# Kernel optimization log

Hardware: AMD Instinct MI355X
Metric: run time of the kernel (lower is better)

Reference implementation:

```python
import jax, jax.numpy as jnp
import numpy as np

N = 50000
E = 640000
F_IN = 128
HID = 128
OUT = 64


def setup_inputs() -> dict:
    key = jax.random.key(0)
    ks = jax.random.split(key, 16)
    x = jax.random.normal(ks[0], (N, F_IN), dtype=jnp.float32)
    edge_index = jax.random.randint(ks[1], (2, E), 0, N, dtype=jnp.int64)

    def lin(k, fan_in, fan_out):
        bound = 1.0 / np.sqrt(fan_in)
        kw, kb = jax.random.split(k)
        W = jax.random.uniform(kw, (fan_in, fan_out), jnp.float32, -bound, bound)
        b = jax.random.uniform(kb, (fan_out,), jnp.float32, -bound, bound)
        return W, b

    W1, b1 = lin(ks[2], F_IN, HID)
    W2, b2 = lin(ks[3], HID, HID)
    W3, b3 = lin(ks[4], HID, HID)
    Wres, bres = lin(ks[5], F_IN, HID)
    Wlin, blin = lin(ks[6], HID, OUT)
    return {"x": x, "edge_index": edge_index,
            "W1": W1, "b1": b1, "W2": W2, "b2": b2, "W3": W3, "b3": b3,
            "Wres": Wres, "bres": bres, "Wlin": Wlin, "blin": blin}


def _gcn_norm(edge_index, n):
    # GCNConv default: add self-loops, symmetric normalization D^-1/2 (A+I) D^-1/2
    src, dst = edge_index[0], edge_index[1]
    deg = jax.ops.segment_sum(jnp.ones((edge_index.shape[1],), jnp.float32), dst,
                              num_segments=n) + 1.0  # +1 for self-loop
    dinv = jax.lax.rsqrt(deg)
    norm_e = dinv[src] * dinv[dst]          # [E] edge coefficients
    norm_self = 1.0 / deg                    # [N] self-loop coefficients
    return src, dst, norm_e, norm_self


def _gcn_conv(x, W, b, src, dst, norm_e, norm_self, n):
    h = x @ W                                # [N, F_out]
    agg = jax.ops.segment_sum(h[src] * norm_e[:, None], dst, num_segments=n)
    agg = agg + h * norm_self[:, None]       # self-loop contribution
    return agg + b


def reference(x, edge_index, W1, b1, W2, b2, W3, b3, Wres, bres, Wlin, blin):
    n = x.shape[0]
    src, dst, norm_e, norm_self = _gcn_norm(edge_index, n)
    x_res = x @ Wres + bres
    h = _gcn_conv(x, W1, b1, src, dst, norm_e, norm_self, n)
    h = jax.nn.relu(h + x_res)               # dropout is identity in eval mode
    h = _gcn_conv(h, W2, b2, src, dst, norm_e, norm_self, n)
    h = jax.nn.relu(h)
    h = _gcn_conv(h, W3, b3, src, dst, norm_e, norm_self, n)
    h = jax.nn.relu(h)
    return h @ Wlin + blin
```

## Files before the change

### kernel.cpp

```cpp
#include <hip/hip_runtime.h>

typedef unsigned short ushort_t;
typedef unsigned int uint_t;

typedef __bf16 bf16x8 __attribute__((ext_vector_type(8)));
typedef float f32x4 __attribute__((ext_vector_type(4)));

union BFU { ushort_t u; __bf16 h; };

__device__ __forceinline__ float bf2f(uint_t u) {
    union { uint_t i; float f; } v; v.i = u << 16; return v.f;
}
__device__ __forceinline__ ushort_t f2bf(float f) {
    union { float f; uint_t i; } v; v.f = f;
    uint_t r = v.i + 0x7fffu + ((v.i >> 16) & 1u);
    return (ushort_t)(r >> 16);
}
__device__ __forceinline__ float loadF(const void* p, size_t i, int isBf16) {
    return isBf16 ? bf2f((uint_t)((const ushort_t*)p)[i]) : ((const float*)p)[i];
}

struct DetectArgs {
    const void* t[11];
    int elems[11];
    const int* ei;
    int* flags;
};

__global__ void k_init(DetectArgs a, int* __restrict__ deg, int n) {
    int i = blockIdx.x * blockDim.x + threadIdx.x;
    if (i < n) deg[i] = 0;
    if (blockIdx.x == 0) {
        int t = threadIdx.x;
        if (t < 11) {
            const uint_t* w = (const uint_t*)a.t[t];
            int m = a.elems[t] / 2; if (m > 64) m = 64;
            int cnt = 0;
            for (int k = 0; k < m; ++k) {
                uint_t field = (w[k] >> 7) & 0xFFu;
                cnt += (field >= 100u && field <= 135u);
            }
            a.flags[t] = (cnt * 10 >= m * 6) ? 1 : 0;
        } else if (t == 11) {
            int nz = 0;
            for (int k = 0; k < 64; ++k) nz += (a.ei[2 * k + 1] != 0);
            a.flags[11] = (nz == 0) ? 1 : 0;
        }
    }
}

__global__ void k_deg(const int* __restrict__ ei, int E, int N,
                      const int* __restrict__ flags, int* __restrict__ deg) {
    int i = blockIdx.x * blockDim.x + threadIdx.x;
    int e0 = i * 4;
    if (e0 >= E) return;
    int is64 = flags[11];
    if (e0 + 3 < E && (E & 3) == 0) {
        int d[4];
        if (is64) {
            int4 va = *(const int4*)(ei + 2 * E + 2 * e0);
            int4 vb = *(const int4*)(ei + 2 * E + 2 * e0 + 4);
            d[0] = va.x; d[1] = va.z; d[2] = vb.x; d[3] = vb.z;
        } else {
            int4 va = *(const int4*)(ei + E + e0);
            d[0] = va.x; d[1] = va.y; d[2] = va.z; d[3] = va.w;
        }
#pragma unroll
        for (int k = 0; k < 4; ++k)
            if ((unsigned)d[k] < (unsigned)N) atomicAdd(&deg[d[k]], 1);
    } else {
        for (int e = e0; e < E && e < e0 + 4; ++e) {
            int dd = is64 ? ei[2 * E + 2 * e] : ei[E + e];
            if ((unsigned)dd < (unsigned)N) atomicAdd(&deg[dd], 1);
        }
    }
}


__global__ __launch_bounds__(256) void k_bsum(const int* __restrict__ deg, int n,
                                              int* __restrict__ bsum) {
    int base = blockIdx.x * 1024;
    int local = 0;
#pragma unroll
    for (int j = 0; j < 4; ++j) {
        int idx = base + threadIdx.x + j * 256;
        if (idx < n) local += deg[idx];
    }
    __shared__ int s[4];
#pragma unroll
    for (int off = 32; off; off >>= 1) local += __shfl_down(local, off, 64);
    if ((threadIdx.x & 63) == 0) s[threadIdx.x >> 6] = local;
    __syncthreads();
    if (threadIdx.x == 0) bsum[blockIdx.x] = s[0] + s[1] + s[2] + s[3];
}

__global__ __launch_bounds__(256) void k_bscan(int* __restrict__ bsum, int nb) {
    __shared__ int s[256];
    int t = threadIdx.x;
    int v = (t < nb) ? bsum[t] : 0;
    s[t] = v;
    __syncthreads();
    for (int off = 1; off < 256; off <<= 1) {
        int u = (t >= off) ? s[t - off] : 0;
        __syncthreads();
        s[t] += u;
        __syncthreads();
    }
    if (t < nb) bsum[t] = s[t] - v;
}

__global__ __launch_bounds__(256) void k_rowptr(const int* __restrict__ deg,
                                                const int* __restrict__ boff, int n,
                                                int* __restrict__ row_ptr,
                                                int* __restrict__ cnt,
                                                float* __restrict__ dinv,
                                                float* __restrict__ nself) {
    __shared__ int s[256];
    int t = threadIdx.x;
    int base = blockIdx.x * 1024 + t * 4;
    int v0 = (base + 0 < n) ? deg[base + 0] : 0;
    int v1 = (base + 1 < n) ? deg[base + 1] : 0;
    int v2 = (base + 2 < n) ? deg[base + 2] : 0;
    int v3 = (base + 3 < n) ? deg[base + 3] : 0;
    int tot = v0 + v1 + v2 + v3;
    s[t] = tot;
    __syncthreads();
    for (int off = 1; off < 256; off <<= 1) {
        int u = (t >= off) ? s[t - off] : 0;
        __syncthreads();
        s[t] += u;
        __syncthreads();
    }
    int run = boff[blockIdx.x] + ((t == 0) ? 0 : s[t - 1]);
    int vals[4] = {v0, v1, v2, v3};
#pragma unroll
    for (int j = 0; j < 4; ++j) {
        int idx = base + j;
        if (idx < n) {
            row_ptr[idx] = run;
            cnt[idx] = run;
            run += vals[j];
            float df = (float)vals[j] + 1.0f;
            dinv[idx] = rsqrtf(df);
            nself[idx] = 1.0f / df;
        }
    }
    if (blockIdx.x == gridDim.x - 1 && t == 255) row_ptr[n] = boff[blockIdx.x] + s[255];
}

__global__ void k_fill(const int* __restrict__ ei, int E, int N,
                       const int* __restrict__ flags,
                       int* __restrict__ cnt,
                       const float* __restrict__ dinv,
                       uint2* __restrict__ colwgt) {
    int i = blockIdx.x * blockDim.x + threadIdx.x;
    int e0 = i * 4;
    if (e0 >= E) return;
    int is64 = flags[11];
    if (e0 + 3 < E && (E & 3) == 0) {
        int s[4], d[4];
        if (is64) {
            int4 sa = *(const int4*)(ei + 2 * e0);
            int4 sb = *(const int4*)(ei + 2 * e0 + 4);
            int4 da = *(const int4*)(ei + 2 * E + 2 * e0);
            int4 db = *(const int4*)(ei + 2 * E + 2 * e0 + 4);
            s[0] = sa.x; s[1] = sa.z; s[2] = sb.x; s[3] = sb.z;
            d[0] = da.x; d[1] = da.z; d[2] = db.x; d[3] = db.z;
        } else {
            int4 sa = *(const int4*)(ei + e0);
            int4 da = *(const int4*)(ei + E + e0);
            s[0] = sa.x; s[1] = sa.y; s[2] = sa.z; s[3] = sa.w;
            d[0] = da.x; d[1] = da.y; d[2] = da.z; d[3] = da.w;
        }
        float wv[4]; int pos[4]; int ss[4]; bool ok[4];
#pragma unroll
        for (int k = 0; k < 4; ++k) {
            ok[k] = (unsigned)d[k] < (unsigned)N;
            ss[k] = ((unsigned)s[k] < (unsigned)N) ? s[k] : 0;
        }
#pragma unroll
        for (int k = 0; k < 4; ++k)
            wv[k] = ok[k] ? dinv[ss[k]] * dinv[d[k]] : 0.0f;
#pragma unroll
        for (int k = 0; k < 4; ++k)
            pos[k] = ok[k] ? atomicAdd(&cnt[d[k]], 1) : 0;
#pragma unroll
        for (int k = 0; k < 4; ++k) {
            if (ok[k]) {
                uint2 pk;
                pk.x = (uint_t)ss[k];
                pk.y = __float_as_uint(wv[k]);
                colwgt[pos[k]] = pk;
            }
        }
    } else {
        for (int e = e0; e < E && e < e0 + 4; ++e) {
            int sv = is64 ? ei[2 * e] : ei[e];
            int dv = is64 ? ei[2 * E + 2 * e] : ei[E + e];
            if ((unsigned)dv < (unsigned)N) {
                int pos = atomicAdd(&cnt[dv], 1);
                int ssv = ((unsigned)sv < (unsigned)N) ? sv : 0;
                uint2 pk;
                pk.x = (uint_t)ssv;
                pk.y = __float_as_uint(dinv[ssv] * dinv[dv]);
                colwgt[pos] = pk;
            }
        }
    }
}

__global__ void k_pack(const void* __restrict__ W1, const void* __restrict__ W2,
                       const void* __restrict__ W3, const void* __restrict__ Wr,
                       const void* __restrict__ Wl, const int* __restrict__ flags,
                       ushort_t* __restrict__ Tcat, ushort_t* __restrict__ T2,
                       ushort_t* __restrict__ T3, ushort_t* __restrict__ Tl) {
    int i = blockIdx.x * blockDim.x + threadIdx.x;
    const int SQ = 128 * 128;
    if (i < 4 * SQ) {
        int m = i / SQ, r = i % SQ;
        int k = r / 128, f = r % 128;
        const void* W = (m == 0) ? W1 : (m == 1) ? W2 : (m == 2) ? W3 : Wr;
        int fid = (m == 0) ? 1 : (m == 1) ? 3 : (m == 2) ? 5 : 7;
        ushort_t* T = (m == 0) ? Tcat : (m == 1) ? T2 : (m == 2) ? T3 : (Tcat + SQ);
        T[f * 128 + k] = f2bf(loadF(W, (size_t)k * 128 + f, flags[fid]));
    } else if (i < 4 * SQ + 128 * 64) {
        int r = i - 4 * SQ;
        int k = r / 64, f = r % 64;
        Tl[f * 128 + k] = f2bf(loadF(Wl, (size_t)k * 64 + f, flags[9]));
    }
}


template <int NCT>
__device__ __forceinline__ void stage_B(const ushort_t* __restrict__ WT, uint4* lds) {
    int t = threadIdx.x;
#pragma unroll
    for (int i = 0; i < NCT; ++i) {
        int g = i * 256 + t;
        uint4 v = ((const uint4*)WT)[g];
        int col = g >> 4, k8 = g & 15;
        int c = col >> 4, l16c = col & 15;
        int kk = k8 >> 2, q = k8 & 3;
        lds[((kk * NCT + c) << 6) + (q << 4) + l16c] = v;
    }
    __syncthreads();
}

__device__ __forceinline__ void load_A2(const void* __restrict__ A, int a16,
                                        int ar0, int ar1, int quad,
                                        bf16x8 afrag[2][4]) {
    if (a16) {
        const ushort_t* p0 = (const ushort_t*)A + (size_t)ar0 * 128 + quad * 8;
        const ushort_t* p1 = (const ushort_t*)A + (size_t)ar1 * 128 + quad * 8;
#pragma unroll
        for (int kk = 0; kk < 4; ++kk) {
            afrag[0][kk] = *(const bf16x8*)(p0 + kk * 32);
            afrag[1][kk] = *(const bf16x8*)(p1 + kk * 32);
        }
    } else {
        const float* p0 = (const float*)A + (size_t)ar0 * 128 + quad * 8;
        const float* p1 = (const float*)A + (size_t)ar1 * 128 + quad * 8;
#pragma unroll
        for (int kk = 0; kk < 4; ++kk) {
            f32x4 u0 = *(const f32x4*)(p0 + kk * 32);
            f32x4 u1 = *(const f32x4*)(p0 + kk * 32 + 4);
            f32x4 v0 = *(const f32x4*)(p1 + kk * 32);
            f32x4 v1 = *(const f32x4*)(p1 + kk * 32 + 4);
#pragma unroll
            for (int j = 0; j < 4; ++j) {
                BFU e;
                e.u = f2bf(u0[j]); afrag[0][kk][j] = e.h;
                e.u = f2bf(u1[j]); afrag[0][kk][j + 4] = e.h;
                e.u = f2bf(v0[j]); afrag[1][kk][j] = e.h;
                e.u = f2bf(v1[j]); afrag[1][kk][j + 4] = e.h;
            }
        }
    }
}

template <int NCT>
__global__ __launch_bounds__(256, 2) void k_gemm2(const void* __restrict__ A, int aFid, int aFix,
                                                  const ushort_t* __restrict__ WT,
                                                  const void* __restrict__ bias, int bFid,
                                                  void* __restrict__ C, int cFix,
                                                  int M, const int* __restrict__ flags) {
    __shared__ uint4 lds[NCT * 256];
    stage_B<NCT>(WT, lds);

    const int F = NCT * 16;
    int t = threadIdx.x;
    int wave = t >> 6, lane = t & 63;
    int quad = lane >> 4, l16 = lane & 15;
    int rowBase = blockIdx.x * 128 + wave * 32;

    int a16 = (aFid >= 0) ? flags[aFid] : aFix;
    int ar0 = rowBase + l16;      if (ar0 >= M) ar0 = M - 1;
    int ar1 = rowBase + 16 + l16; if (ar1 >= M) ar1 = M - 1;

    bf16x8 afrag[2][4];
    load_A2(A, a16, ar0, ar1, quad, afrag);

    f32x4 acc[2][NCT];
#pragma unroll
    for (int r = 0; r < 2; ++r)
#pragma unroll
        for (int c = 0; c < NCT; ++c) acc[r][c] = (f32x4){0.f, 0.f, 0.f, 0.f};

#pragma unroll
    for (int kk = 0; kk < 4; ++kk) {
#pragma unroll
        for (int c = 0; c < NCT; ++c) {
            bf16x8 b = *(const bf16x8*)&lds[((kk * NCT + c) << 6) + lane];
            acc[0][c] = __builtin_amdgcn_mfma_f32_16x16x32_bf16(afrag[0][kk], b, acc[0][c], 0, 0, 0);
            acc[1][c] = __builtin_amdgcn_mfma_f32_16x16x32_bf16(afrag[1][kk], b, acc[1][c], 0, 0, 0);
        }
    }

    int bf = (bias && bFid >= 0) ? flags[bFid] : 1;
#pragma unroll
    for (int r = 0; r < 2; ++r) {
#pragma unroll
        for (int c = 0; c < NCT; ++c) {
            int colg = c * 16 + l16;
            float bv = bias ? loadF(bias, colg, bf) : 0.0f;
#pragma unroll
            for (int q = 0; q < 4; ++q) {
                int row = rowBase + r * 16 + quad * 4 + q;
                if (row < M) {
                    float v = acc[r][c][q] + bv;
                    if (cFix) ((ushort_t*)C)[(size_t)row * F + colg] = f2bf(v);
                    else      ((float*)C)[(size_t)row * F + colg] = v;
                }
            }
        }
    }
}

__global__ __launch_bounds__(256, 1) void k_gemm_l1(const void* __restrict__ A,
                                                    const ushort_t* __restrict__ Tcat,
                                                    const void* __restrict__ bres,
                                                    ushort_t* __restrict__ Hout,
                                                    float* __restrict__ Xres,
                                                    int M, const int* __restrict__ flags) {
    __shared__ uint4 lds[16 * 256];
    stage_B<16>(Tcat, lds);

    int t = threadIdx.x;
    int wave = t >> 6, lane = t & 63;
    int quad = lane >> 4, l16 = lane & 15;
    int rowBase = blockIdx.x * 128 + wave * 32;

    int a16 = flags[0];
    int ar0 = rowBase + l16;      if (ar0 >= M) ar0 = M - 1;
    int ar1 = rowBase + 16 + l16; if (ar1 >= M) ar1 = M - 1;

    bf16x8 afrag[2][4];
    load_A2(A, a16, ar0, ar1, quad, afrag);

    f32x4 acc[2][16];
#pragma unroll
    for (int r = 0; r < 2; ++r)
#pragma unroll
        for (int c = 0; c < 16; ++c) acc[r][c] = (f32x4){0.f, 0.f, 0.f, 0.f};

#pragma unroll
    for (int kk = 0; kk < 4; ++kk) {
#pragma unroll
        for (int c = 0; c < 16; ++c) {
            bf16x8 b = *(const bf16x8*)&lds[((kk * 16 + c) << 6) + lane];
            acc[0][c] = __builtin_amdgcn_mfma_f32_16x16x32_bf16(afrag[0][kk], b, acc[0][c], 0, 0, 0);
            acc[1][c] = __builtin_amdgcn_mfma_f32_16x16x32_bf16(afrag[1][kk], b, acc[1][c], 0, 0, 0);
        }
    }

    int bf = flags[8];
#pragma unroll
    for (int r = 0; r < 2; ++r) {
#pragma unroll
        for (int c = 0; c < 16; ++c) {
            int colg = c * 16 + l16;
            float bv = (c >= 8) ? loadF(bres, colg - 128, bf) : 0.0f;
#pragma unroll
            for (int q = 0; q < 4; ++q) {
                int row = rowBase + r * 16 + quad * 4 + q;
                if (row < M) {
                    float v = acc[r][c][q] + bv;
                    if (c < 8) Hout[(size_t)row * 128 + colg] = f2bf(v);
                    else       Xres[(size_t)row * 128 + (colg - 128)] = v;
                }
            }
        }
    }
}

__global__ __launch_bounds__(256) void k_agg(const ushort_t* __restrict__ H,
                                             const int* __restrict__ row_ptr,
                                             const uint2* __restrict__ colwgt,
                                             const float* __restrict__ nself,
                                             const void* __restrict__ bias, int bFid,
                                             const float* __restrict__ other,
                                             ushort_t* __restrict__ Out,
                                             int n, const int* __restrict__ flags) {
    int node = (blockIdx.x * blockDim.x + threadIdx.x) >> 6;
    if (node >= n) return;
    int lane = threadIdx.x & 63;
    int f = lane * 2;

    float ns = nself[node];
    size_t nidx = (size_t)node * 128 + f;

    uint_t hv = *(const uint_t*)(H + nidx);
    float a0 = bf2f(hv & 0xffffu) * ns;
    float a1 = bf2f(hv >> 16) * ns;

    int beg = row_ptr[node], end = row_ptr[node + 1];
    for (int bs = beg; bs < end; bs += 64) {
        int rem = end - bs;
        int nb = (rem < 64) ? rem : 64;
        uint2 m = (lane < nb) ? colwgt[bs + lane] : (uint2){0u, 0u};
        int c = (int)m.x;
        float w = __uint_as_float(m.y);

        for (int j = 0; j < nb; j += 16) {
            int si[16]; float wi[16]; uint_t vi[16];
#pragma unroll
            for (int q = 0; q < 16; ++q) {
                si[q] = __shfl(c, j + q, 64);
                wi[q] = __shfl(w, j + q, 64);
            }
#pragma unroll
            for (int q = 0; q < 16; ++q)
                vi[q] = *(const uint_t*)(H + (size_t)si[q] * 128 + f);
#pragma unroll
            for (int q = 0; q < 16; ++q) {
                a0 = fmaf(bf2f(vi[q] & 0xffffu), wi[q], a0);
                a1 = fmaf(bf2f(vi[q] >> 16), wi[q], a1);
            }
        }
    }

    int bfm = flags[bFid];
    a0 += loadF(bias, f, bfm);
    a1 += loadF(bias, f + 1, bfm);
    if (other) {
        a0 += other[nidx];
        a1 += other[nidx + 1];
    }
    a0 = fmaxf(a0, 0.0f);
    a1 = fmaxf(a1, 0.0f);
    uint_t outv = (uint_t)f2bf(a0) | ((uint_t)f2bf(a1) << 16);
    *(uint_t*)(Out + nidx) = outv;
}


extern "C" void kernel_launch(void* const* d_in, const int* in_sizes, int n_in,
                              void* d_out, int out_size, void* d_ws, size_t ws_size,
                              hipStream_t stream) {
    const int N = in_sizes[0] / 128;
    const int E = in_sizes[1] / 2;

    const void* x  = d_in[0];
    const int*  ei = (const int*)d_in[1];

    char* ws = (char*)d_ws;
    size_t used = 0;
    auto alloc = [&](size_t bytes) {
        char* p = ws + used;
        used += (bytes + 255) & ~(size_t)255;
        return p;
    };

    int*   flags   = (int*)alloc(64 * 4);
    int*   deg     = (int*)alloc((size_t)N * 4);
    int*   cnt     = (int*)alloc((size_t)N * 4);
    int*   row_ptr = (int*)alloc((size_t)(N + 1) * 4);
    float* dinv    = (float*)alloc((size_t)N * 4);
    float* nself   = (float*)alloc((size_t)N * 4);
    uint2* colwgt  = (uint2*)alloc((size_t)E * 8);
    int*   bsum    = (int*)alloc(256 * 4);
    ushort_t* Tcat = (ushort_t*)alloc(256 * 128 * 2);
    ushort_t* T2   = (ushort_t*)alloc(128 * 128 * 2);
    ushort_t* T3   = (ushort_t*)alloc(128 * 128 * 2);
    ushort_t* Tlin = (ushort_t*)alloc(128 * 64 * 2);

    ushort_t* Hbuf = (ushort_t*)alloc((size_t)N * 128 * 2);
    ushort_t* Act1 = (ushort_t*)alloc((size_t)N * 128 * 2);
    ushort_t* Act2 = (ushort_t*)alloc((size_t)N * 128 * 2);
    float*    Xres = (float*)alloc((size_t)N * 128 * 4);

    if (used > ws_size) return;

    DetectArgs da;
    for (int i = 0; i < 11; ++i) { da.t[i] = d_in[i == 0 ? 0 : i + 1]; da.elems[i] = in_sizes[i == 0 ? 0 : i + 1]; }
    da.ei = ei;
    da.flags = flags;

    const int B = 256;
    int gInit = (N + B - 1) / B;
    int gE4   = ((E + 3) / 4 + B - 1) / B;
    int gPack = (4 * 128 * 128 + 128 * 64 + B - 1) / B;
    int gGemm = (N + 127) / 128;
    int gAgg  = (N + 3) / 4;
    int nb    = (N + 1023) / 1024;

    k_init<<<gInit, B, 0, stream>>>(da, deg, N);
    k_pack<<<gPack, B, 0, stream>>>(d_in[2], d_in[4], d_in[6], d_in[8], d_in[10], flags,
                                    Tcat, T2, T3, Tlin);
    k_deg<<<gE4, B, 0, stream>>>(ei, E, N, flags, deg);
    k_bsum<<<nb, B, 0, stream>>>(deg, N, bsum);
    k_bscan<<<1, B, 0, stream>>>(bsum, nb);
    k_rowptr<<<nb, B, 0, stream>>>(deg, bsum, N, row_ptr, cnt, dinv, nself);
    k_fill<<<gE4, B, 0, stream>>>(ei, E, N, flags, cnt, dinv, colwgt);

    k_gemm_l1<<<gGemm, B, 0, stream>>>(x, Tcat, d_in[9], Hbuf, Xres, N, flags);
    k_agg<<<gAgg, B, 0, stream>>>(Hbuf, row_ptr, colwgt, nself, d_in[3], 2,
                                  Xres, Act1, N, flags);

    k_gemm2<8><<<gGemm, B, 0, stream>>>(Act1, -1, 1, T2, nullptr, -1, Hbuf, 1, N, flags);
    k_agg<<<gAgg, B, 0, stream>>>(Hbuf, row_ptr, colwgt, nself, d_in[5], 4,
                                  nullptr, Act2, N, flags);

    k_gemm2<8><<<gGemm, B, 0, stream>>>(Act2, -1, 1, T3, nullptr, -1, Hbuf, 1, N, flags);
    k_agg<<<gAgg, B, 0, stream>>>(Hbuf, row_ptr, colwgt, nself, d_in[7], 6,
                                  nullptr, Act1, N, flags);

    k_gemm2<4><<<gGemm, B, 0, stream>>>(Act1, -1, 1, Tlin, d_in[11], 10,
                                        d_out, 0, N, flags);
}
```

Baseline: 351.3 us.

## Capture per-edge slot in degree pass and store residual in bf16

The degree-count kernel now keeps the value returned by its atomic increment as each edge's local slot. It writes (dst, slot) to a temporary array, so the CSR fill becomes an atomic-free scatter at row_ptr[dst]+slot, and the separate cnt array is dropped. Separately, the residual projection Xres is stored as bf16 instead of fp32, halving its write and read traffic. The cost is an extra E*8-byte temporary buffer plus its write and read, and lower precision in the residual addition.

```diff
diff --git a/kernel.cpp b/kernel.cpp
--- a/kernel.cpp
+++ b/kernel.cpp
@@ -50,7 +50,8 @@
 }
 
 __global__ void k_deg(const int* __restrict__ ei, int E, int N,
-                      const int* __restrict__ flags, int* __restrict__ deg) {
+                      const int* __restrict__ flags, int* __restrict__ deg,
+                      int2* __restrict__ tmp) {
     int i = blockIdx.x * blockDim.x + threadIdx.x;
     int e0 = i * 4;
     if (e0 >= E) return;
@@ -65,13 +66,25 @@
             int4 va = *(const int4*)(ei + E + e0);
             d[0] = va.x; d[1] = va.y; d[2] = va.z; d[3] = va.w;
         }
+        int l[4]; bool ok[4];
+#pragma unroll
+        for (int k = 0; k < 4; ++k) ok[k] = (unsigned)d[k] < (unsigned)N;
 #pragma unroll
         for (int k = 0; k < 4; ++k)
-            if ((unsigned)d[k] < (unsigned)N) atomicAdd(&deg[d[k]], 1);
+            l[k] = ok[k] ? atomicAdd(&deg[d[k]], 1) : 0;
+        int4 t01, t23;
+        t01.x = ok[0] ? d[0] : -1; t01.y = l[0];
+        t01.z = ok[1] ? d[1] : -1; t01.w = l[1];
+        t23.x = ok[2] ? d[2] : -1; t23.y = l[2];
+        t23.z = ok[3] ? d[3] : -1; t23.w = l[3];
+        *(int4*)(tmp + e0) = t01;
+        *(int4*)(tmp + e0 + 2) = t23;
     } else {
         for (int e = e0; e < E && e < e0 + 4; ++e) {
             int dd = is64 ? ei[2 * E + 2 * e] : ei[E + e];
-            if ((unsigned)dd < (unsigned)N) atomicAdd(&deg[dd], 1);
+            bool ok = (unsigned)dd < (unsigned)N;
+            int l = ok ? atomicAdd(&deg[dd], 1) : 0;
+            tmp[e] = make_int2(ok ? dd : -1, l);
         }
     }
 }
@@ -112,7 +125,6 @@
 __global__ __launch_bounds__(256) void k_rowptr(const int* __restrict__ deg,
                                                 const int* __restrict__ boff, int n,
                                                 int* __restrict__ row_ptr,
-                                                int* __restrict__ cnt,
                                                 float* __restrict__ dinv,
                                                 float* __restrict__ nself) {
     __shared__ int s[256];
@@ -138,7 +150,6 @@
         int idx = base + j;
         if (idx < n) {
             row_ptr[idx] = run;
-            cnt[idx] = run;
             run += vals[j];
             float df = (float)vals[j] + 1.0f;
             dinv[idx] = rsqrtf(df);
@@ -148,45 +159,44 @@
     if (blockIdx.x == gridDim.x - 1 && t == 255) row_ptr[n] = boff[blockIdx.x] + s[255];
 }
 
-__global__ void k_fill(const int* __restrict__ ei, int E, int N,
-                       const int* __restrict__ flags,
-                       int* __restrict__ cnt,
-                       const float* __restrict__ dinv,
-                       uint2* __restrict__ colwgt) {
+__global__ void k_scatter(const int* __restrict__ ei, int E, int N,
+                          const int* __restrict__ flags,
+                          const int* __restrict__ row_ptr,
+                          const float* __restrict__ dinv,
+                          const int2* __restrict__ tmp,
+                          uint2* __restrict__ colwgt) {
     int i = blockIdx.x * blockDim.x + threadIdx.x;
     int e0 = i * 4;
     if (e0 >= E) return;
     int is64 = flags[11];
     if (e0 + 3 < E && (E & 3) == 0) {
-        int s[4], d[4];
+        int s[4];
         if (is64) {
             int4 sa = *(const int4*)(ei + 2 * e0);
             int4 sb = *(const int4*)(ei + 2 * e0 + 4);
-            int4 da = *(const int4*)(ei + 2 * E + 2 * e0);
-            int4 db = *(const int4*)(ei + 2 * E + 2 * e0 + 4);
             s[0] = sa.x; s[1] = sa.z; s[2] = sb.x; s[3] = sb.z;
-            d[0] = da.x; d[1] = da.z; d[2] = db.x; d[3] = db.z;
         } else {
             int4 sa = *(const int4*)(ei + e0);
-            int4 da = *(const int4*)(ei + E + e0);
             s[0] = sa.x; s[1] = sa.y; s[2] = sa.z; s[3] = sa.w;
-            d[0] = da.x; d[1] = da.y; d[2] = da.z; d[3] = da.w;
-        }
-        float wv[4]; int pos[4]; int ss[4]; bool ok[4];
+        }
+        int4 t01 = *(const int4*)(tmp + e0);
+        int4 t23 = *(const int4*)(tmp + e0 + 2);
+        int d[4] = {t01.x, t01.z, t23.x, t23.z};
+        int l[4] = {t01.y, t01.w, t23.y, t23.w};
+        int ss[4]; int pos[4]; float wv[4];
+#pragma unroll
+        for (int k = 0; k < 4; ++k)
+            ss[k] = ((unsigned)s[k] < (unsigned)N) ? s[k] : 0;
 #pragma unroll
         for (int k = 0; k < 4; ++k) {
-            ok[k] = (unsigned)d[k] < (unsigned)N;
-            ss[k] = ((unsigned)s[k] < (unsigned)N) ? s[k] : 0;
-        }
-#pragma unroll
-        for (int k = 0; k < 4; ++k)
-            wv[k] = ok[k] ? dinv[ss[k]] * dinv[d[k]] : 0.0f;
-#pragma unroll
-        for (int k = 0; k < 4; ++k)
-            pos[k] = ok[k] ? atomicAdd(&cnt[d[k]], 1) : 0;
+            if (d[k] >= 0) {
+                pos[k] = row_ptr[d[k]] + l[k];
+                wv[k] = dinv[ss[k]] * dinv[d[k]];
+            }
+        }
 #pragma unroll
         for (int k = 0; k < 4; ++k) {
-            if (ok[k]) {
+            if (d[k] >= 0) {
                 uint2 pk;
                 pk.x = (uint_t)ss[k];
                 pk.y = __float_as_uint(wv[k]);
@@ -196,14 +206,13 @@
     } else {
         for (int e = e0; e < E && e < e0 + 4; ++e) {
             int sv = is64 ? ei[2 * e] : ei[e];
-            int dv = is64 ? ei[2 * E + 2 * e] : ei[E + e];
-            if ((unsigned)dv < (unsigned)N) {
-                int pos = atomicAdd(&cnt[dv], 1);
+            int2 tv = tmp[e];
+            if (tv.x >= 0) {
                 int ssv = ((unsigned)sv < (unsigned)N) ? sv : 0;
                 uint2 pk;
                 pk.x = (uint_t)ssv;
-                pk.y = __float_as_uint(dinv[ssv] * dinv[dv]);
-                colwgt[pos] = pk;
+                pk.y = __float_as_uint(dinv[ssv] * dinv[tv.x]);
+                colwgt[row_ptr[tv.x] + tv.y] = pk;
             }
         }
     }
@@ -340,7 +349,7 @@
                                                     const ushort_t* __restrict__ Tcat,
                                                     const void* __restrict__ bres,
                                                     ushort_t* __restrict__ Hout,
-                                                    float* __restrict__ Xres,
+                                                    ushort_t* __restrict__ Xres,
                                                     int M, const int* __restrict__ flags) {
     __shared__ uint4 lds[16 * 256];
     stage_B<16>(Tcat, lds);
@@ -386,7 +395,7 @@
                 if (row < M) {
                     float v = acc[r][c][q] + bv;
                     if (c < 8) Hout[(size_t)row * 128 + colg] = f2bf(v);
-                    else       Xres[(size_t)row * 128 + (colg - 128)] = v;
+                    else       Xres[(size_t)row * 128 + (colg - 128)] = f2bf(v);
                 }
             }
         }
@@ -398,7 +407,7 @@
                                              const uint2* __restrict__ colwgt,
                                              const float* __restrict__ nself,
                                              const void* __restrict__ bias, int bFid,
-                                             const float* __restrict__ other,
+                                             const ushort_t* __restrict__ other,
                                              ushort_t* __restrict__ Out,
                                              int n, const int* __restrict__ flags) {
     int node = (blockIdx.x * blockDim.x + threadIdx.x) >> 6;
@@ -443,8 +452,9 @@
     a0 += loadF(bias, f, bfm);
     a1 += loadF(bias, f + 1, bfm);
     if (other) {
-        a0 += other[nidx];
-        a1 += other[nidx + 1];
+        uint_t ov = *(const uint_t*)(other + nidx);
+        a0 += bf2f(ov & 0xffffu);
+        a1 += bf2f(ov >> 16);
     }
     a0 = fmaxf(a0, 0.0f);
     a1 = fmaxf(a1, 0.0f);
@@ -472,10 +482,10 @@
 
     int*   flags   = (int*)alloc(64 * 4);
     int*   deg     = (int*)alloc((size_t)N * 4);
-    int*   cnt     = (int*)alloc((size_t)N * 4);
     int*   row_ptr = (int*)alloc((size_t)(N + 1) * 4);
     float* dinv    = (float*)alloc((size_t)N * 4);
     float* nself   = (float*)alloc((size_t)N * 4);
+    int2*  tmp     = (int2*)alloc((size_t)E * 8);
     uint2* colwgt  = (uint2*)alloc((size_t)E * 8);
     int*   bsum    = (int*)alloc(256 * 4);
     ushort_t* Tcat = (ushort_t*)alloc(256 * 128 * 2);
@@ -486,7 +496,7 @@
     ushort_t* Hbuf = (ushort_t*)alloc((size_t)N * 128 * 2);
     ushort_t* Act1 = (ushort_t*)alloc((size_t)N * 128 * 2);
     ushort_t* Act2 = (ushort_t*)alloc((size_t)N * 128 * 2);
-    float*    Xres = (float*)alloc((size_t)N * 128 * 4);
+    ushort_t* Xres = (ushort_t*)alloc((size_t)N * 128 * 2);
 
     if (used > ws_size) return;
 
@@ -506,11 +516,11 @@
     k_init<<<gInit, B, 0, stream>>>(da, deg, N);
     k_pack<<<gPack, B, 0, stream>>>(d_in[2], d_in[4], d_in[6], d_in[8], d_in[10], flags,
                                     Tcat, T2, T3, Tlin);
-    k_deg<<<gE4, B, 0, stream>>>(ei, E, N, flags, deg);
+    k_deg<<<gE4, B, 0, stream>>>(ei, E, N, flags, deg, tmp);
     k_bsum<<<nb, B, 0, stream>>>(deg, N, bsum);
     k_bscan<<<1, B, 0, stream>>>(bsum, nb);
-    k_rowptr<<<nb, B, 0, stream>>>(deg, bsum, N, row_ptr, cnt, dinv, nself);
-    k_fill<<<gE4, B, 0, stream>>>(ei, E, N, flags, cnt, dinv, colwgt);
+    k_rowptr<<<nb, B, 0, stream>>>(deg, bsum, N, row_ptr, dinv, nself);
+    k_scatter<<<gE4, B, 0, stream>>>(ei, E, N, flags, row_ptr, dinv, tmp, colwgt);
 
     k_gemm_l1<<<gGemm, B, 0, stream>>>(x, Tcat, d_in[9], Hbuf, Xres, N, flags);
     k_agg<<<gAgg, B, 0, stream>>>(Hbuf, row_ptr, colwgt, nself, d_in[3], 2,
```

Result: faster. 331.7 us (-5.6%).
